# Performance work log

Hardware: AMD Instinct MI355X
Metric: run time of the kernel (lower is better)

## Reference

```python
import jax, jax.numpy as jnp
import numpy as np

N, H, MSG, OUT = 512, 128, 128, 64
F1, F2 = 256, 256  # f_dims (also used for g_mlp per source)
GOUT = 128         # hardcoded output_gmlp_dim
O1 = 256           # o_dims


def _p(key, shape, scale):
    return jax.random.normal(key, shape, dtype=jnp.float32) * scale


def setup_inputs() -> dict:
    key = jax.random.key(0)
    ks = jax.random.split(key, 24)
    s = lambda fan_in: 1.0 / np.sqrt(fan_in)
    inp = {
        "x": jax.random.normal(ks[0], (N, H), dtype=jnp.float32),
        "hidden": jax.random.normal(ks[1], (N, H), dtype=jnp.float32),
        "h0": jnp.zeros((1, N, H), dtype=jnp.float32),
        "c0": jnp.zeros((1, N, H), dtype=jnp.float32),
        # f MLP: 2H -> F1 -> F2 -> MSG
        "Wf1": _p(ks[2], (F1, 2 * H), s(2 * H)), "bf1": jnp.zeros((F1,), jnp.float32),
        "Wf2": _p(ks[3], (F2, F1), s(F1)), "bf2": jnp.zeros((F2,), jnp.float32),
        "Wf3": _p(ks[4], (MSG, F2), s(F2)), "bf3": jnp.zeros((MSG,), jnp.float32),
        # g_mlp: H+MSG -> F1 -> F2 -> GOUT
        "Wg1": _p(ks[5], (F1, H + MSG), s(H + MSG)), "bg1": jnp.zeros((F1,), jnp.float32),
        "Wg2": _p(ks[6], (F2, F1), s(F1)), "bg2": jnp.zeros((F2,), jnp.float32),
        "Wg3": _p(ks[7], (GOUT, F2), s(F2)), "bg3": jnp.zeros((GOUT,), jnp.float32),
        # LSTM (1 layer): GOUT -> H, gate order i,f,g,o
        "W_ih": _p(ks[8], (4 * H, GOUT), s(H)), "W_hh": _p(ks[9], (4 * H, H), s(H)),
        "b_ih": jnp.zeros((4 * H,), jnp.float32), "b_hh": jnp.zeros((4 * H,), jnp.float32),
        # o MLP: H -> O1 -> OUT
        "Wo1": _p(ks[10], (O1, H), s(H)), "bo1": jnp.zeros((O1,), jnp.float32),
        "Wo2": _p(ks[11], (OUT, O1), s(O1)), "bo2": jnp.zeros((OUT,), jnp.float32),
    }
    return inp


def reference(x, hidden, h0, c0,
              Wf1, bf1, Wf2, bf2, Wf3, bf3,
              Wg1, bg1, Wg2, bg2, Wg3, bg3,
              W_ih, W_hh, b_ih, b_hh,
              Wo1, bo1, Wo2, bo2):
    # --- pairwise message MLP f(cat(hidden[i], hidden[j])) over all (i,j) ---
    # split first-layer weight to avoid materializing [N,N,2H] concat
    A = hidden @ Wf1[:, :H].T            # [N, F1], contribution of node i
    B = hidden @ Wf1[:, H:].T            # [N, F1], contribution of node j
    h1 = jax.nn.relu(A[:, None, :] + B[None, :, :] + bf1)   # [N, N, F1]
    h2 = jax.nn.relu(h1 @ Wf2.T + bf2)                       # [N, N, F2]
    messages = h2 @ Wf3.T + bf3                              # [N, N, MSG]
    sum_messages = jnp.sum(messages, axis=0)                 # [N, MSG] (sum over i)

    # --- g_mlp on cat(x, sum_messages) ---
    g_in = jnp.concatenate([x, sum_messages], axis=1)        # [N, H+MSG]
    g1 = jax.nn.relu(g_in @ Wg1.T + bg1)
    g2 = jax.nn.relu(g1 @ Wg2.T + bg2)
    input_g = g2 @ Wg3.T + bg3                               # [N, GOUT]

    # --- single-step LSTM (seq_len=1, batch=N), PyTorch gate order i,f,g,o ---
    gates = input_g @ W_ih.T + b_ih + h0[0] @ W_hh.T + b_hh  # [N, 4H]
    i_g, f_g, g_g, o_g = jnp.split(gates, 4, axis=1)
    i_g = jax.nn.sigmoid(i_g); f_g = jax.nn.sigmoid(f_g)
    g_g = jnp.tanh(g_g); o_g = jax.nn.sigmoid(o_g)
    c_new = f_g * c0[0] + i_g * g_g
    hidden_new = o_g * jnp.tanh(c_new)                       # [N, H]

    # --- output MLP o (single_output=False) ---
    o1 = jax.nn.relu(hidden_new @ Wo1.T + bo1)
    out = o1 @ Wo2.T + bo2                                   # [N, OUT]

    return (out, hidden_new, hidden_new[None], c_new[None])
```

## Files before the change

kernel.cpp:

```cpp
#include <hip/hip_runtime.h>
#include <hip/hip_bf16.h>


#define NN   512
#define HH   128
#define F1D  256
#define F2D  256
#define OUTD 64
#define ICHUNK 64

typedef _Float16 half_t;
typedef _Float16 half8 __attribute__((ext_vector_type(8)));
typedef float float4_t __attribute__((ext_vector_type(4)));
typedef float float8_t __attribute__((ext_vector_type(8)));

__device__ __forceinline__ float sigmoidf_(float x) {
    return 1.0f / (1.0f + __expf(-x));
}

#define HL_INV 2.44140625e-4f

#define WS_TAIL_B 1835008
#define T3H 0
#define G1H 65536
#define G2H 196608
#define G3H 327680
#define CATH 393216
#define O1H 655360
#define O2H 720896

__constant__ int p_cum[8]   = {16, 24, 40, 56, 64, 96, 112, 116};
__constant__ int p_K[8]     = {256, 256, 256, 256, 256, 256, 128, 256};
__constant__ int p_hioff[8] = {0, T3H, G1H, G2H, G3H, CATH, O1H, O2H};
__constant__ int p_cnt[8]   = {65536, 32768, 65536, 65536, 32768, 131072, 32768, 16384};

__global__ __launch_bounds__(256)
void kP_prep(const float* __restrict__ hidden,
             const float* __restrict__ Wf1,
             const float* __restrict__ bf1,
             const float* __restrict__ Wf2,
             const float* __restrict__ Wf3,
             const float* __restrict__ Wg1, const float* __restrict__ Wg2,
             const float* __restrict__ Wg3,
             const float* __restrict__ W_ih, const float* __restrict__ W_hh,
             const float* __restrict__ Wo1, const float* __restrict__ Wo2,
             half_t* __restrict__ tail,
             half_t* __restrict__ W2H, half_t* __restrict__ W2L,
             float* __restrict__ A32, float* __restrict__ B32,
             float* __restrict__ S) {
    __shared__ float slab[4096];
    const int t = threadIdx.x;
    const int bid = blockIdx.x;

    if (bid < 116) {
        int m = 0;
        while (m < 7 && bid >= p_cum[m]) ++m;
        const int pl = bid - (m ? p_cum[m - 1] : 0);
        const int K = p_K[m];
        const int kshift = (K == 256) ? 8 : 7;
        const int n0 = pl * 16;

        const float* src;
        switch (m) {
            case 0: src = Wf2; break;
            case 1: src = Wf3; break;
            case 2: src = Wg1; break;
            case 3: src = Wg2; break;
            case 4: src = Wg3; break;
            case 6: src = Wo1; break;
            default: src = Wo2; break;
        }
        for (int q = t; q < (16 * K) / 4; q += 256) {
            const int flat = q * 4;
            const int r = flat >> kshift;
            const int k = flat & (K - 1);
            float4_t v;
            if (m == 5) {
                v = (k < 128) ? *(const float4_t*)(W_ih + (n0 + r) * 128 + k)
                              : *(const float4_t*)(W_hh + (n0 + r) * 128 + (k - 128));
            } else {
                v = *(const float4_t*)(src + (size_t)(n0 + r) * K + k);
            }
            *(float4_t*)&slab[flat] = v;
        }
        __syncthreads();

        half_t *hi, *lo;
        if (m == 0) { hi = W2H; lo = W2L; }
        else        { hi = tail + p_hioff[m]; lo = hi + p_cnt[m]; }
        const int base = pl * (K << 4);
        for (int f0 = t * 8; f0 < 16 * K; f0 += 2048) {
            const int ks = f0 >> 9;
            const int g4 = (f0 >> 7) & 3;
            const int l15 = (f0 >> 3) & 15;
            const int k0 = ks * 32 + g4 * 8;
            float8_t v = *(const float8_t*)&slab[l15 * K + k0];
            half8 hv, lv;
#pragma unroll
            for (int e = 0; e < 8; ++e) {
                half_t h = (half_t)v[e];
                hv[e] = h;
                lv[e] = (half_t)((v[e] - (float)h) * 4096.0f);
            }
            *(half8*)(hi + base + f0) = hv;
            *(half8*)(lo + base + f0) = lv;
        }
    } else {
        const int pb = bid - 116;
        const int i0 = pb * 4;

        {
            float4_t z = {0.0f, 0.0f, 0.0f, 0.0f};
            *(float4_t*)(S + (size_t)pb * 1024 + t * 4) = z;
        }

        float* hid = slab;
        for (int q = t; q < 4 * HH; q += 256)
            hid[q] = hidden[i0 * HH + q];
        __syncthreads();

        float accA[4], accB[4];
        const float b = bf1[t];
#pragma unroll
        for (int r = 0; r < 4; ++r) { accA[r] = b; accB[r] = 0.0f; }

        const float* wr = Wf1 + t * 256;
#pragma unroll 4
        for (int k = 0; k < HH; k += 4) {
            float4_t wa = *(const float4_t*)(wr + k);
            float4_t wb = *(const float4_t*)(wr + HH + k);
#pragma unroll
            for (int r = 0; r < 4; ++r) {
                const float* hp = &hid[r * HH + k];
                accA[r] += wa[0]*hp[0] + wa[1]*hp[1] + wa[2]*hp[2] + wa[3]*hp[3];
                accB[r] += wb[0]*hp[0] + wb[1]*hp[1] + wb[2]*hp[2] + wb[3]*hp[3];
            }
        }
#pragma unroll
        for (int r = 0; r < 4; ++r) {
            A32[(i0 + r) * F1D + t] = accA[r];
            B32[(i0 + r) * F1D + t] = accB[r];
        }
    }
}

__global__ __launch_bounds__(512, 2)
void k2_pairwise(const float* __restrict__ A32,
                 const float* __restrict__ B32,
                 const half_t* __restrict__ W2H,
                 const half_t* __restrict__ W2L,
                 const float* __restrict__ bf2,
                 float* __restrict__ S) {
    __shared__ half_t hbuf[2][4][8][512];

    const int tid = threadIdx.x;
    const int lane = tid & 63;
    const int w = tid >> 6;
    const int l15 = lane & 15;
    const int g4 = lane >> 4;
    const int j0 = blockIdx.y * 16;
    const int i0 = blockIdx.x * ICHUNK;
    const int lane8 = lane * 8;

    const half8* WH8 = (const half8*)W2H;
    const half8* WL8 = (const half8*)W2L;
    half8 Wh[2][8], Wl[2][8];
#pragma unroll
    for (int nt = 0; nt < 2; ++nt)
#pragma unroll
        for (int ks = 0; ks < 8; ++ks) {
            const int idx = (w * 2 + nt) * 512 + ks * 64 + lane;
            Wh[nt][ks] = WH8[idx];
            Wl[nt][ks] = WL8[idx];
        }
#pragma unroll
    for (int nt = 0; nt < 2; ++nt)
#pragma unroll
        for (int ks = 0; ks < 8; ++ks) {
            asm volatile("" : "+v"(Wh[nt][ks]));
            asm volatile("" : "+v"(Wl[nt][ks]));
        }

    float4_t Bw0 = *(const float4_t*)(B32 + (size_t)(j0 + l15) * F1D + w * 32 + g4 * 8);
    float4_t Bw1 = *(const float4_t*)(B32 + (size_t)(j0 + l15) * F1D + w * 32 + g4 * 8 + 4);

    float b2v[2];
#pragma unroll
    for (int nt = 0; nt < 2; ++nt) b2v[nt] = bf2[w * 32 + nt * 16 + l15];

    float4_t acc[2];
#pragma unroll
    for (int nt = 0; nt < 2; ++nt)
#pragma unroll
        for (int r = 0; r < 4; ++r) acc[nt][r] = 0.0f;

#pragma unroll
    for (int q = 0; q < 4; ++q) {
        const float* Ap = A32 + (size_t)(i0 + q) * F1D + w * 32 + g4 * 8;
        float4_t a0 = *(const float4_t*)Ap;
        float4_t a1 = *(const float4_t*)(Ap + 4);
        half8 hf;
#pragma unroll
        for (int e = 0; e < 4; ++e) {
            hf[e]     = (half_t)fmaxf(a0[e] + Bw0[e], 0.0f);
            hf[4 + e] = (half_t)fmaxf(a1[e] + Bw1[e], 0.0f);
        }
        *(half8*)&hbuf[0][q][w][lane8] = hf;
    }
    __syncthreads();

    for (int c = 0; c < 16; ++c) {
        const int cur = c & 1;
        const int nxt = cur ^ 1;
        const int ibase = i0 + (c + 1) * 4;

#pragma unroll
        for (int q = 0; q < 4; ++q) {
            float4_t a0, a1;
            if (c < 15) {
                const float* Ap = A32 + (size_t)(ibase + q) * F1D + w * 32 + g4 * 8;
                a0 = *(const float4_t*)Ap;
                a1 = *(const float4_t*)(Ap + 4);
            }

            float4_t C[2], Cl[2];
#pragma unroll
            for (int nt = 0; nt < 2; ++nt)
#pragma unroll
                for (int r = 0; r < 4; ++r) { C[nt][r] = 0.0f; Cl[nt][r] = 0.0f; }
#pragma unroll
            for (int ks = 0; ks < 8; ++ks) {
                half8 hf = *(const half8*)&hbuf[cur][q][ks][lane8];
                C[0]  = __builtin_amdgcn_mfma_f32_16x16x32_f16(hf, Wh[0][ks], C[0], 0, 0, 0);
                C[1]  = __builtin_amdgcn_mfma_f32_16x16x32_f16(hf, Wh[1][ks], C[1], 0, 0, 0);
                Cl[0] = __builtin_amdgcn_mfma_f32_16x16x32_f16(hf, Wl[0][ks], Cl[0], 0, 0, 0);
                Cl[1] = __builtin_amdgcn_mfma_f32_16x16x32_f16(hf, Wl[1][ks], Cl[1], 0, 0, 0);
            }

            if (c < 15) {
                half8 hf;
#pragma unroll
                for (int e = 0; e < 4; ++e) {
                    hf[e]     = (half_t)fmaxf(a0[e] + Bw0[e], 0.0f);
                    hf[4 + e] = (half_t)fmaxf(a1[e] + Bw1[e], 0.0f);
                }
                *(half8*)&hbuf[nxt][q][w][lane8] = hf;
            }

#pragma unroll
            for (int nt = 0; nt < 2; ++nt)
#pragma unroll
                for (int r = 0; r < 4; ++r) {
                    float v = fmaf(Cl[nt][r], HL_INV, C[nt][r]) + b2v[nt];
                    acc[nt][r] += fmaxf(v, 0.0f);
                }
        }
        __syncthreads();
    }

#pragma unroll
    for (int nt = 0; nt < 2; ++nt)
#pragma unroll
        for (int r = 0; r < 4; ++r)
            atomicAdd(&S[(size_t)(j0 + g4 * 4 + r) * F2D + w * 32 + nt * 16 + l15], acc[nt][r]);
}

#define AST 260

template<int NT, int NKS>
__device__ __forceinline__ void frag_gemm(const float* __restrict__ aPtr,
                                          const half_t* __restrict__ WhF,
                                          const half_t* __restrict__ WlF,
                                          const int* pB, int lane8,
                                          float4_t* Chi, float4_t* Clo) {
#pragma unroll
    for (int ks = 0; ks < NKS; ++ks) {
        float4_t a0 = *(const float4_t*)(aPtr + ks * 32);
        float4_t a1 = *(const float4_t*)(aPtr + ks * 32 + 4);
        half8 ah, al;
#pragma unroll
        for (int e = 0; e < 4; ++e) {
            half_t h0 = (half_t)a0[e];
            ah[e] = h0; al[e] = (half_t)((a0[e] - (float)h0) * 4096.0f);
            half_t h1 = (half_t)a1[e];
            ah[4+e] = h1; al[4+e] = (half_t)((a1[e] - (float)h1) * 4096.0f);
        }
#pragma unroll
        for (int nt = 0; nt < NT; ++nt) {
            half8 wh = *(const half8*)(WhF + pB[nt] + ks * 512 + lane8);
            half8 wl = *(const half8*)(WlF + pB[nt] + ks * 512 + lane8);
            Chi[nt] = __builtin_amdgcn_mfma_f32_16x16x32_f16(ah, wh, Chi[nt], 0, 0, 0);
            Clo[nt] = __builtin_amdgcn_mfma_f32_16x16x32_f16(ah, wl, Clo[nt], 0, 0, 0);
            Clo[nt] = __builtin_amdgcn_mfma_f32_16x16x32_f16(al, wh, Clo[nt], 0, 0, 0);
        }
    }
}

__global__ __launch_bounds__(512)
void k4_tail(const float* __restrict__ S,
             const float* __restrict__ x,
             const float* __restrict__ h0,
             const float* __restrict__ c0,
             const half_t* __restrict__ tail,
             const float* __restrict__ bf3,
             const float* __restrict__ bg1, const float* __restrict__ bg2,
             const float* __restrict__ bg3,
             const float* __restrict__ b_ih, const float* __restrict__ b_hh,
             const float* __restrict__ bo1, const float* __restrict__ bo2,
             float* __restrict__ out,
             float* __restrict__ hid_out,
             float* __restrict__ h_out,
             float* __restrict__ c_out) {
    __shared__ float bufA[16 * AST];
    __shared__ float bufB[16 * AST];
    __shared__ float bufC[16 * AST];
    const int tid = threadIdx.x;
    const int lane = tid & 63;
    const int w = tid >> 6;
    const int l15 = lane & 15;
    const int g4 = lane >> 4;
    const int r0 = blockIdx.x * 16;
    const int lane8 = lane * 8;

    for (int q = tid; q < 16 * 256; q += 512)
        bufC[(q >> 8) * AST + (q & 255)] = S[(size_t)(r0 + (q >> 8)) * 256 + (q & 255)];
    for (int q = tid; q < 16 * 128; q += 512)
        bufA[(q >> 7) * AST + (q & 127)] = x[(r0 + (q >> 7)) * 128 + (q & 127)];
    __syncthreads();

    const float* aFrag;
    int pB[4];
    float4_t Chi[4], Clo[4];

    {
        const int n = w * 16 + l15;
        pB[0] = w * 4096;
        Chi[0] = float4_t{0,0,0,0}; Clo[0] = float4_t{0,0,0,0};
        aFrag = bufC + l15 * AST + g4 * 8;
        frag_gemm<1, 8>(aFrag, tail + T3H, tail + T3H + 32768, pB, lane8, Chi, Clo);
        const float b = 512.0f * bf3[n];
#pragma unroll
        for (int r = 0; r < 4; ++r)
            bufA[(g4 * 4 + r) * AST + 128 + n] = Chi[0][r] + Clo[0][r] * HL_INV + b;
    }
    __syncthreads();

    {
        pB[0] = (w * 2) * 4096; pB[1] = (w * 2 + 1) * 4096;
        Chi[0] = float4_t{0,0,0,0}; Clo[0] = float4_t{0,0,0,0};
        Chi[1] = float4_t{0,0,0,0}; Clo[1] = float4_t{0,0,0,0};
        aFrag = bufA + l15 * AST + g4 * 8;
        frag_gemm<2, 8>(aFrag, tail + G1H, tail + G1H + 65536, pB, lane8, Chi, Clo);
#pragma unroll
        for (int nt = 0; nt < 2; ++nt) {
            const int n = w * 32 + nt * 16 + l15;
            const float b = bg1[n];
#pragma unroll
            for (int r = 0; r < 4; ++r)
                bufB[(g4 * 4 + r) * AST + n] = fmaxf(Chi[nt][r] + Clo[nt][r] * HL_INV + b, 0.0f);
        }
    }
    __syncthreads();

    {
        pB[0] = (w * 2) * 4096; pB[1] = (w * 2 + 1) * 4096;
        Chi[0] = float4_t{0,0,0,0}; Clo[0] = float4_t{0,0,0,0};
        Chi[1] = float4_t{0,0,0,0}; Clo[1] = float4_t{0,0,0,0};
        aFrag = bufB + l15 * AST + g4 * 8;
        frag_gemm<2, 8>(aFrag, tail + G2H, tail + G2H + 65536, pB, lane8, Chi, Clo);
#pragma unroll
        for (int nt = 0; nt < 2; ++nt) {
            const int n = w * 32 + nt * 16 + l15;
            const float b = bg2[n];
#pragma unroll
            for (int r = 0; r < 4; ++r)
                bufC[(g4 * 4 + r) * AST + n] = fmaxf(Chi[nt][r] + Clo[nt][r] * HL_INV + b, 0.0f);
        }
        for (int q = tid; q < 16 * 128; q += 512)
            bufA[(q >> 7) * AST + 128 + (q & 127)] = h0[(r0 + (q >> 7)) * 128 + (q & 127)];
    }
    __syncthreads();

    {
        const int n = w * 16 + l15;
        pB[0] = w * 4096;
        Chi[0] = float4_t{0,0,0,0}; Clo[0] = float4_t{0,0,0,0};
        aFrag = bufC + l15 * AST + g4 * 8;
        frag_gemm<1, 8>(aFrag, tail + G3H, tail + G3H + 32768, pB, lane8, Chi, Clo);
        const float b = bg3[n];
#pragma unroll
        for (int r = 0; r < 4; ++r)
            bufA[(g4 * 4 + r) * AST + n] = Chi[0][r] + Clo[0][r] * HL_INV + b;
    }
    __syncthreads();

    {
#pragma unroll
        for (int nt = 0; nt < 4; ++nt) {
            pB[nt] = (w + nt * 8) * 4096;
            Chi[nt] = float4_t{0,0,0,0}; Clo[nt] = float4_t{0,0,0,0};
        }
        aFrag = bufA + l15 * AST + g4 * 8;
        frag_gemm<4, 8>(aFrag, tail + CATH, tail + CATH + 131072, pB, lane8, Chi, Clo);

        const int nh = w * 16 + l15;
        float bi = b_ih[nh]       + b_hh[nh];
        float bf = b_ih[128 + nh] + b_hh[128 + nh];
        float bg = b_ih[256 + nh] + b_hh[256 + nh];
        float bo = b_ih[384 + nh] + b_hh[384 + nh];
#pragma unroll
        for (int r = 0; r < 4; ++r) {
            const int row = r0 + g4 * 4 + r;
            float gi = sigmoidf_(Chi[0][r] + Clo[0][r] * HL_INV + bi);
            float gf = sigmoidf_(Chi[1][r] + Clo[1][r] * HL_INV + bf);
            float gg = tanhf(    Chi[2][r] + Clo[2][r] * HL_INV + bg);
            float go = sigmoidf_(Chi[3][r] + Clo[3][r] * HL_INV + bo);
            float c = gf * c0[row * 128 + nh] + gi * gg;
            float h = go * tanhf(c);
            bufC[(g4 * 4 + r) * AST + nh] = h;
            hid_out[row * 128 + nh] = h;
            h_out[row * 128 + nh]   = h;
            c_out[row * 128 + nh]   = c;
        }
    }
    __syncthreads();

    {
        pB[0] = (w * 2) * 2048; pB[1] = (w * 2 + 1) * 2048;
        Chi[0] = float4_t{0,0,0,0}; Clo[0] = float4_t{0,0,0,0};
        Chi[1] = float4_t{0,0,0,0}; Clo[1] = float4_t{0,0,0,0};
        aFrag = bufC + l15 * AST + g4 * 8;
        frag_gemm<2, 4>(aFrag, tail + O1H, tail + O1H + 32768, pB, lane8, Chi, Clo);
#pragma unroll
        for (int nt = 0; nt < 2; ++nt) {
            const int n = w * 32 + nt * 16 + l15;
            const float b = bo1[n];
#pragma unroll
            for (int r = 0; r < 4; ++r)
                bufB[(g4 * 4 + r) * AST + n] = fmaxf(Chi[nt][r] + Clo[nt][r] * HL_INV + b, 0.0f);
        }
    }
    __syncthreads();

    if (w < 4) {
        const int n = w * 16 + l15;
        pB[0] = w * 4096;
        Chi[0] = float4_t{0,0,0,0}; Clo[0] = float4_t{0,0,0,0};
        aFrag = bufB + l15 * AST + g4 * 8;
        frag_gemm<1, 8>(aFrag, tail + O2H, tail + O2H + 16384, pB, lane8, Chi, Clo);
        const float b = bo2[n];
#pragma unroll
        for (int r = 0; r < 4; ++r)
            out[(r0 + g4 * 4 + r) * OUTD + n] = Chi[0][r] + Clo[0][r] * HL_INV + b;
    }
}

extern "C" void kernel_launch(void* const* d_in, const int* in_sizes, int n_in,
                              void* d_out, int out_size, void* d_ws, size_t ws_size,
                              hipStream_t stream) {
    const float* x      = (const float*)d_in[0];
    const float* hidden = (const float*)d_in[1];
    const float* h0     = (const float*)d_in[2];
    const float* c0     = (const float*)d_in[3];
    const float* Wf1    = (const float*)d_in[4];
    const float* bf1    = (const float*)d_in[5];
    const float* Wf2    = (const float*)d_in[6];
    const float* bf2    = (const float*)d_in[7];
    const float* Wf3    = (const float*)d_in[8];
    const float* bf3    = (const float*)d_in[9];
    const float* Wg1    = (const float*)d_in[10];
    const float* bg1    = (const float*)d_in[11];
    const float* Wg2    = (const float*)d_in[12];
    const float* bg2    = (const float*)d_in[13];
    const float* Wg3    = (const float*)d_in[14];
    const float* bg3    = (const float*)d_in[15];
    const float* W_ih   = (const float*)d_in[16];
    const float* W_hh   = (const float*)d_in[17];
    const float* b_ih   = (const float*)d_in[18];
    const float* b_hh   = (const float*)d_in[19];
    const float* Wo1    = (const float*)d_in[20];
    const float* bo1    = (const float*)d_in[21];
    const float* Wo2    = (const float*)d_in[22];
    const float* bo2    = (const float*)d_in[23];

    char* wsb = (char*)d_ws;
    float*  A32  = (float*)(wsb + 0);
    float*  B32  = (float*)(wsb + 524288);
    half_t* W2H  = (half_t*)(wsb + 1048576);
    half_t* W2L  = (half_t*)(wsb + 1179648);
    float*  S    = (float*)(wsb + 1310720);
    half_t* tail = (half_t*)(wsb + WS_TAIL_B);

    float* outp  = (float*)d_out;
    float* hid1  = (float*)d_out + 32768;
    float* hid2  = (float*)d_out + 98304;
    float* cout  = (float*)d_out + 163840;

    kP_prep<<<dim3(244), dim3(256), 0, stream>>>(hidden, Wf1, bf1, Wf2,
                                                 Wf3, Wg1, Wg2, Wg3,
                                                 W_ih, W_hh, Wo1, Wo2,
                                                 tail, W2H, W2L,
                                                 A32, B32, S);

    k2_pairwise<<<dim3(8, 32), dim3(512), 0, stream>>>(A32, B32, W2H, W2L, bf2, S);

    k4_tail<<<dim3(32), dim3(512), 0, stream>>>(S, x, h0, c0, tail,
                                                bf3, bg1, bg2, bg3,
                                                b_ih, b_hh, bo1, bo2,
                                                outp, hid1, hid2, cout);
}
```

Baseline: 197.3 us.

## Pack four prep jobs per block and widen tail kernel to sixteen waves

The prep kernel now runs four 256-thread sub-jobs per 1024-thread block, cutting the grid from 244 to 61 blocks. The tail kernel doubles to 16 waves, so each wave computes fewer output tiles per GEMM stage. The LSTM gate pre-activations are staged through a new shared buffer so the pointwise cell update can run on all threads. This aims to shorten the serial latency of the small tail GEMMs, at the cost of more shared memory, an extra barrier, and block-wide syncs in prep that now span unrelated sub-jobs.

After: 250.7 us. 1.27x slower.

```diff
diff --git a/kernel.cpp b/kernel.cpp
--- a/kernel.cpp
+++ b/kernel.cpp
@@ -34,7 +34,7 @@
 __constant__ int p_hioff[8] = {0, T3H, G1H, G2H, G3H, CATH, O1H, O2H};
 __constant__ int p_cnt[8]   = {65536, 32768, 65536, 65536, 32768, 131072, 32768, 16384};
 
-__global__ __launch_bounds__(256)
+__global__ __launch_bounds__(1024)
 void kP_prep(const float* __restrict__ hidden,
              const float* __restrict__ Wf1,
              const float* __restrict__ bf1,
@@ -48,14 +48,17 @@
              half_t* __restrict__ W2H, half_t* __restrict__ W2L,
              float* __restrict__ A32, float* __restrict__ B32,
              float* __restrict__ S) {
-    __shared__ float slab[4096];
-    const int t = threadIdx.x;
-    const int bid = blockIdx.x;
-
-    if (bid < 116) {
+    __shared__ float slab[4][4096];
+    const int tid = threadIdx.x;
+    const int sub = tid >> 8;
+    const int t = tid & 255;
+    const int jb = blockIdx.x * 4 + sub;
+    float* mySlab = slab[sub];
+
+    if (jb < 116) {
         int m = 0;
-        while (m < 7 && bid >= p_cum[m]) ++m;
-        const int pl = bid - (m ? p_cum[m - 1] : 0);
+        while (m < 7 && jb >= p_cum[m]) ++m;
+        const int pl = jb - (m ? p_cum[m - 1] : 0);
         const int K = p_K[m];
         const int kshift = (K == 256) ? 8 : 7;
         const int n0 = pl * 16;
@@ -81,7 +84,7 @@
             } else {
                 v = *(const float4_t*)(src + (size_t)(n0 + r) * K + k);
             }
-            *(float4_t*)&slab[flat] = v;
+            *(float4_t*)&mySlab[flat] = v;
         }
         __syncthreads();
 
@@ -94,7 +97,7 @@
             const int g4 = (f0 >> 7) & 3;
             const int l15 = (f0 >> 3) & 15;
             const int k0 = ks * 32 + g4 * 8;
-            float8_t v = *(const float8_t*)&slab[l15 * K + k0];
+            float8_t v = *(const float8_t*)&mySlab[l15 * K + k0];
             half8 hv, lv;
 #pragma unroll
             for (int e = 0; e < 8; ++e) {
@@ -106,7 +109,7 @@
             *(half8*)(lo + base + f0) = lv;
         }
     } else {
-        const int pb = bid - 116;
+        const int pb = jb - 116;
         const int i0 = pb * 4;
 
         {
@@ -114,7 +117,7 @@
             *(float4_t*)(S + (size_t)pb * 1024 + t * 4) = z;
         }
 
-        float* hid = slab;
+        float* hid = mySlab;
         for (int q = t; q < 4 * HH; q += 256)
             hid[q] = hidden[i0 * HH + q];
         __syncthreads();
@@ -296,7 +299,7 @@
     }
 }
 
-__global__ __launch_bounds__(512)
+__global__ __launch_bounds__(1024)
 void k4_tail(const float* __restrict__ S,
              const float* __restrict__ x,
              const float* __restrict__ h0,
@@ -314,6 +317,7 @@
     __shared__ float bufA[16 * AST];
     __shared__ float bufB[16 * AST];
     __shared__ float bufC[16 * AST];
+    __shared__ float gt[16][512];
     const int tid = threadIdx.x;
     const int lane = tid & 63;
     const int w = tid >> 6;
@@ -322,17 +326,17 @@
     const int r0 = blockIdx.x * 16;
     const int lane8 = lane * 8;
 
-    for (int q = tid; q < 16 * 256; q += 512)
+    for (int q = tid; q < 16 * 256; q += 1024)
         bufC[(q >> 8) * AST + (q & 255)] = S[(size_t)(r0 + (q >> 8)) * 256 + (q & 255)];
-    for (int q = tid; q < 16 * 128; q += 512)
+    for (int q = tid; q < 16 * 128; q += 1024)
         bufA[(q >> 7) * AST + (q & 127)] = x[(r0 + (q >> 7)) * 128 + (q & 127)];
     __syncthreads();
 
     const float* aFrag;
-    int pB[4];
-    float4_t Chi[4], Clo[4];
-
-    {
+    int pB[2];
+    float4_t Chi[2], Clo[2];
+
+    if (w < 8) {
         const int n = w * 16 + l15;
         pB[0] = w * 4096;
         Chi[0] = float4_t{0,0,0,0}; Clo[0] = float4_t{0,0,0,0};
@@ -346,42 +350,34 @@
     __syncthreads();
 
     {
-        pB[0] = (w * 2) * 4096; pB[1] = (w * 2 + 1) * 4096;
+        const int n = w * 16 + l15;
+        pB[0] = w * 4096;
         Chi[0] = float4_t{0,0,0,0}; Clo[0] = float4_t{0,0,0,0};
-        Chi[1] = float4_t{0,0,0,0}; Clo[1] = float4_t{0,0,0,0};
         aFrag = bufA + l15 * AST + g4 * 8;
-        frag_gemm<2, 8>(aFrag, tail + G1H, tail + G1H + 65536, pB, lane8, Chi, Clo);
-#pragma unroll
-        for (int nt = 0; nt < 2; ++nt) {
-            const int n = w * 32 + nt * 16 + l15;
-            const float b = bg1[n];
-#pragma unroll
-            for (int r = 0; r < 4; ++r)
-                bufB[(g4 * 4 + r) * AST + n] = fmaxf(Chi[nt][r] + Clo[nt][r] * HL_INV + b, 0.0f);
-        }
+        frag_gemm<1, 8>(aFrag, tail + G1H, tail + G1H + 65536, pB, lane8, Chi, Clo);
+        const float b = bg1[n];
+#pragma unroll
+        for (int r = 0; r < 4; ++r)
+            bufB[(g4 * 4 + r) * AST + n] = fmaxf(Chi[0][r] + Clo[0][r] * HL_INV + b, 0.0f);
     }
     __syncthreads();
 
     {
-        pB[0] = (w * 2) * 4096; pB[1] = (w * 2 + 1) * 4096;
+        const int n = w * 16 + l15;
+        pB[0] = w * 4096;
         Chi[0] = float4_t{0,0,0,0}; Clo[0] = float4_t{0,0,0,0};
-        Chi[1] = float4_t{0,0,0,0}; Clo[1] = float4_t{0,0,0,0};
         aFrag = bufB + l15 * AST + g4 * 8;
-        frag_gemm<2, 8>(aFrag, tail + G2H, tail + G2H + 65536, pB, lane8, Chi, Clo);
-#pragma unroll
-        for (int nt = 0; nt < 2; ++nt) {
-            const int n = w * 32 + nt * 16 + l15;
-            const float b = bg2[n];
-#pragma unroll
-            for (int r = 0; r < 4; ++r)
-                bufC[(g4 * 4 + r) * AST + n] = fmaxf(Chi[nt][r] + Clo[nt][r] * HL_INV + b, 0.0f);
-        }
-        for (int q = tid; q < 16 * 128; q += 512)
+        frag_gemm<1, 8>(aFrag, tail + G2H, tail + G2H + 65536, pB, lane8, Chi, Clo);
+        const float b = bg2[n];
+#pragma unroll
+        for (int r = 0; r < 4; ++r)
+            bufC[(g4 * 4 + r) * AST + n] = fmaxf(Chi[0][r] + Clo[0][r] * HL_INV + b, 0.0f);
+        for (int q = tid; q < 16 * 128; q += 1024)
             bufA[(q >> 7) * AST + 128 + (q & 127)] = h0[(r0 + (q >> 7)) * 128 + (q & 127)];
     }
     __syncthreads();
 
-    {
+    if (w < 8) {
         const int n = w * 16 + l15;
         pB[0] = w * 4096;
         Chi[0] = float4_t{0,0,0,0}; Clo[0] = float4_t{0,0,0,0};
@@ -396,28 +392,37 @@
 
     {
 #pragma unroll
-        for (int nt = 0; nt < 4; ++nt) {
-            pB[nt] = (w + nt * 8) * 4096;
+        for (int nt = 0; nt < 2; ++nt) {
+            pB[nt] = (w * 2 + nt) * 4096;
             Chi[nt] = float4_t{0,0,0,0}; Clo[nt] = float4_t{0,0,0,0};
         }
         aFrag = bufA + l15 * AST + g4 * 8;
-        frag_gemm<4, 8>(aFrag, tail + CATH, tail + CATH + 131072, pB, lane8, Chi, Clo);
-
-        const int nh = w * 16 + l15;
-        float bi = b_ih[nh]       + b_hh[nh];
-        float bf = b_ih[128 + nh] + b_hh[128 + nh];
-        float bg = b_ih[256 + nh] + b_hh[256 + nh];
-        float bo = b_ih[384 + nh] + b_hh[384 + nh];
-#pragma unroll
-        for (int r = 0; r < 4; ++r) {
-            const int row = r0 + g4 * 4 + r;
-            float gi = sigmoidf_(Chi[0][r] + Clo[0][r] * HL_INV + bi);
-            float gf = sigmoidf_(Chi[1][r] + Clo[1][r] * HL_INV + bf);
-            float gg = tanhf(    Chi[2][r] + Clo[2][r] * HL_INV + bg);
-            float go = sigmoidf_(Chi[3][r] + Clo[3][r] * HL_INV + bo);
+        frag_gemm<2, 8>(aFrag, tail + CATH, tail + CATH + 131072, pB, lane8, Chi, Clo);
+#pragma unroll
+        for (int nt = 0; nt < 2; ++nt) {
+            const int n = w * 32 + nt * 16 + l15;
+            const float b = b_ih[n] + b_hh[n];
+#pragma unroll
+            for (int r = 0; r < 4; ++r)
+                gt[g4 * 4 + r][n] = Chi[nt][r] + Clo[nt][r] * HL_INV + b;
+        }
+    }
+    __syncthreads();
+
+    {
+        const int nh = tid & 127;
+        const int rb = tid >> 7;
+#pragma unroll
+        for (int rr = 0; rr < 2; ++rr) {
+            const int r = rb + rr * 8;
+            const int row = r0 + r;
+            float gi = sigmoidf_(gt[r][nh]);
+            float gf = sigmoidf_(gt[r][128 + nh]);
+            float gg = tanhf(    gt[r][256 + nh]);
+            float go = sigmoidf_(gt[r][384 + nh]);
             float c = gf * c0[row * 128 + nh] + gi * gg;
             float h = go * tanhf(c);
-            bufC[(g4 * 4 + r) * AST + nh] = h;
+            bufC[r * AST + nh] = h;
             hid_out[row * 128 + nh] = h;
             h_out[row * 128 + nh]   = h;
             c_out[row * 128 + nh]   = c;
@@ -426,19 +431,15 @@
     __syncthreads();
 
     {
-        pB[0] = (w * 2) * 2048; pB[1] = (w * 2 + 1) * 2048;
+        const int n = w * 16 + l15;
+        pB[0] = w * 2048;
         Chi[0] = float4_t{0,0,0,0}; Clo[0] = float4_t{0,0,0,0};
-        Chi[1] = float4_t{0,0,0,0}; Clo[1] = float4_t{0,0,0,0};
         aFrag = bufC + l15 * AST + g4 * 8;
-        frag_gemm<2, 4>(aFrag, tail + O1H, tail + O1H + 32768, pB, lane8, Chi, Clo);
-#pragma unroll
-        for (int nt = 0; nt < 2; ++nt) {
-            const int n = w * 32 + nt * 16 + l15;
-            const float b = bo1[n];
-#pragma unroll
-            for (int r = 0; r < 4; ++r)
-                bufB[(g4 * 4 + r) * AST + n] = fmaxf(Chi[nt][r] + Clo[nt][r] * HL_INV + b, 0.0f);
-        }
+        frag_gemm<1, 4>(aFrag, tail + O1H, tail + O1H + 32768, pB, lane8, Chi, Clo);
+        const float b = bo1[n];
+#pragma unroll
+        for (int r = 0; r < 4; ++r)
+            bufB[(g4 * 4 + r) * AST + n] = fmaxf(Chi[0][r] + Clo[0][r] * HL_INV + b, 0.0f);
     }
     __syncthreads();
 
@@ -496,7 +497,7 @@
     float* hid2  = (float*)d_out + 98304;
     float* cout  = (float*)d_out + 163840;
 
-    kP_prep<<<dim3(244), dim3(256), 0, stream>>>(hidden, Wf1, bf1, Wf2,
+    kP_prep<<<dim3(61), dim3(1024), 0, stream>>>(hidden, Wf1, bf1, Wf2,
                                                  Wf3, Wg1, Wg2, Wg3,
                                                  W_ih, W_hh, Wo1, Wo2,
                                                  tail, W2H, W2L,
@@ -504,8 +505,8 @@
 
     k2_pairwise<<<dim3(8, 32), dim3(512), 0, stream>>>(A32, B32, W2H, W2L, bf2, S);
 
-    k4_tail<<<dim3(32), dim3(512), 0, stream>>>(S, x, h0, c0, tail,
-                                                bf3, bg1, bg2, bg3,
-                                                b_ih, b_hh, bo1, bo2,
-                                                outp, hid1, hid2, cout);
+    k4_tail<<<dim3(32), dim3(1024), 0, stream>>>(S, x, h0, c0, tail,
+                                                 bf3, bg1, bg2, bg3,
+                                                 b_ih, b_hh, bo1, bo2,
+                                                 outp, hid1, hid2, cout);
 }
```
